# Optimization experiments

Hardware: AMD Instinct MI355X
Metric: run time of the kernel (lower is better)

Reference implementation:

```python
import jax, jax.numpy as jnp
import numpy as np
import itertools

N_SUBSETS = 4
TAU = 0.1


def setup_inputs() -> dict:
    key = jax.random.key(0)
    k1, k2, k3 = jax.random.split(key, 3)
    # scale projections so exp(sim/tau) stays numerically sane (module assumes small/normalized projections)
    projections = jax.random.normal(k1, (8192, 128), dtype=jnp.float32) * 0.05
    xrecon = jax.random.normal(k2, (8192, 784), dtype=jnp.float32)
    recon_label = jax.random.normal(k3, (8192, 784), dtype=jnp.float32)
    return {"projections": projections, "xrecon": xrecon, "recon_label": recon_label}


def _joint_loss(projections, xrecon, recon_label):
    # reconstruction MSE
    recon_loss = jnp.mean(jnp.square(xrecon - recon_label))

    # ---- XNegloss (SimCLR-style with n_subsets positives per group) ----
    N, D = projections.shape
    sim = (projections @ projections.T) / TAU  # [N, N] dot similarity
    gid = jnp.arange(N) // N_SUBSETS
    pos_mask = gid[:, None] == gid[None, :]  # same-group entries are positives
    exp_sim = jnp.exp(sim)
    # original code drops positive entries exactly equal to 1 (positives[positives != 1])
    pos_sum = jnp.sum(jnp.where(pos_mask & (sim != 1.0), exp_sim, 0.0), axis=-1)
    neg_sum = jnp.sum(jnp.where(pos_mask, 0.0, exp_sim), axis=-1)
    closs = jnp.mean(-jnp.log(pos_sum / (pos_sum + neg_sum)))

    # ---- distance loss: MSE over all subset pairs within each group ----
    combi = np.array(list(itertools.combinations(range(N_SUBSETS), 2)))
    left, right = combi[:, 0], combi[:, 1]
    P = projections.reshape(N // N_SUBSETS, N_SUBSETS, D)
    # per-group mean over (pairs, D) then mean over groups == global mean (equal counts)
    dist_loss = jnp.mean(jnp.square(P[:, left] - P[:, right]))

    loss = recon_loss + closs + dist_loss
    return loss, closs, recon_loss, dist_loss


def reference(projections, xrecon, recon_label):
    return _joint_loss(projections, xrecon, recon_label)
```

## Files before the change

### kernel.cpp

```cpp
#include <hip/hip_runtime.h>
#include <hip/hip_bf16.h>
#include <stdint.h>

typedef __bf16 bf16x8 __attribute__((ext_vector_type(8)));
typedef float  f32x4  __attribute__((ext_vector_type(4)));

#define NROWS   8192
#define DIMK    128
#define NGROUPS 2048
#define RECON_N 6422528
#define RECON_N4 (RECON_N / 4)
#define SIM_BLOCKS   512
#define RECON_BLOCKS 1568
#define GROUP_BLOCKS (NGROUPS / 4)
#define FUSED_BLOCKS (SIM_BLOCKS + RECON_BLOCKS + GROUP_BLOCKS)
#define CLOSS_BLOCKS 32

#define LOG2E10 14.4269504088896341f

#define WS_SP     0
#define WS_G      65536
#define WS_E      73728
#define WS_RPART  81920
#define WS_DPART  83488
#define WS_CPART  84000
#define WS_PB     84032

__device__ __forceinline__ unsigned short f2bf(float f) {
    union { __hip_bfloat16 h; unsigned short u; } v;
    v.h = __float2bfloat16(f);
    return v.u;
}

__global__ __launch_bounds__(256) void convert_kernel(const float4* __restrict__ P,
                                                      uint2* __restrict__ out) {
    int idx = blockIdx.x * 256 + threadIdx.x;
    float4 a = P[idx];
    uint2 r;
    r.x = (uint32_t)f2bf(a.x) | ((uint32_t)f2bf(a.y) << 16);
    r.y = (uint32_t)f2bf(a.z) | ((uint32_t)f2bf(a.w) << 16);
    out[idx] = r;
}

__global__ __launch_bounds__(256, 2) void fused_kernel(
        const unsigned short* __restrict__ Pb,
        const float* __restrict__ Pf,
        const float4* __restrict__ X,
        const float4* __restrict__ Y,
        float* __restrict__ ws) {
    const int bx = blockIdx.x;
    const int wave = threadIdx.x >> 6, lane = threadIdx.x & 63;

    if (bx < SIM_BLOCKS) {
        float* Sp = ws + WS_SP;
        __shared__ float sred[2][2][64];
        const int wr = wave >> 1, wc = wave & 1;
        const int rowBase = (bx >> 3) * 128;
        const int colBase = (bx & 7) * 1024;
        const int m = lane & 15, kq = lane >> 4;

        bf16x8 Af[4][4];
#pragma unroll
        for (int i = 0; i < 4; ++i) {
            const unsigned short* rowp =
                Pb + (size_t)(rowBase + wr * 64 + i * 16 + m) * DIMK + kq * 8;
#pragma unroll
            for (int kk = 0; kk < 4; ++kk)
                Af[i][kk] = *(const bf16x8*)(rowp + kk * 32);
        }

        float rowAcc[4][4];
#pragma unroll
        for (int i = 0; i < 4; ++i)
#pragma unroll
            for (int r = 0; r < 4; ++r) rowAcc[i][r] = 0.f;

        for (int t = 0; t < 8; ++t) {
            const unsigned short* bbase =
                Pb + (size_t)(colBase + t * 128 + wc * 64) * DIMK;
#pragma unroll
            for (int j = 0; j < 4; ++j) {
                const unsigned short* bp = bbase + (j * 16 + m) * DIMK + kq * 8;
                bf16x8 Bf[4];
#pragma unroll
                for (int kk = 0; kk < 4; ++kk)
                    Bf[kk] = *(const bf16x8*)(bp + kk * 32);
                f32x4 acc[4];
#pragma unroll
                for (int i = 0; i < 4; ++i) acc[i] = (f32x4){0.f, 0.f, 0.f, 0.f};
#pragma unroll
                for (int kk = 0; kk < 4; ++kk)
#pragma unroll
                    for (int i = 0; i < 4; ++i)
                        acc[i] = __builtin_amdgcn_mfma_f32_16x16x32_bf16(
                            Af[i][kk], Bf[kk], acc[i], 0, 0, 0);
#pragma unroll
                for (int i = 0; i < 4; ++i)
#pragma unroll
                    for (int r = 0; r < 4; ++r)
                        rowAcc[i][r] += exp2f(acc[i][r] * LOG2E10);
            }
        }

#pragma unroll
        for (int i = 0; i < 4; ++i)
#pragma unroll
            for (int r = 0; r < 4; ++r) {
                float sv = rowAcc[i][r];
                sv += __shfl_xor(sv, 1, 64);
                sv += __shfl_xor(sv, 2, 64);
                sv += __shfl_xor(sv, 4, 64);
                sv += __shfl_xor(sv, 8, 64);
                rowAcc[i][r] = sv;
            }
        if ((lane & 15) == 0) {
            int c = lane >> 4;
#pragma unroll
            for (int i = 0; i < 4; ++i)
#pragma unroll
                for (int r = 0; r < 4; ++r)
                    sred[wc][wr][i * 16 + c * 4 + r] = rowAcc[i][r];
        }
        __syncthreads();
        if (wc == 0) {
            float v = sred[0][wr][lane] + sred[1][wr][lane];
            Sp[(size_t)(bx & 7) * NROWS + rowBase + wr * 64 + lane] = v;
        }
    } else if (bx < SIM_BLOCKS + RECON_BLOCKS) {
        __shared__ float red[4];
        int rb = bx - SIM_BLOCKS;
        int base = rb * 1024 + threadIdx.x;
        float4 a0 = X[base], b0 = Y[base];
        float4 a1 = X[base + 256], b1 = Y[base + 256];
        float4 a2 = X[base + 512], b2 = Y[base + 512];
        float4 a3 = X[base + 768], b3 = Y[base + 768];
        float s = 0.f;
        float d;
        d = a0.x - b0.x; s += d * d;  d = a0.y - b0.y; s += d * d;
        d = a0.z - b0.z; s += d * d;  d = a0.w - b0.w; s += d * d;
        d = a1.x - b1.x; s += d * d;  d = a1.y - b1.y; s += d * d;
        d = a1.z - b1.z; s += d * d;  d = a1.w - b1.w; s += d * d;
        d = a2.x - b2.x; s += d * d;  d = a2.y - b2.y; s += d * d;
        d = a2.z - b2.z; s += d * d;  d = a2.w - b2.w; s += d * d;
        d = a3.x - b3.x; s += d * d;  d = a3.y - b3.y; s += d * d;
        d = a3.z - b3.z; s += d * d;  d = a3.w - b3.w; s += d * d;
#pragma unroll
        for (int mm = 1; mm < 64; mm <<= 1) s += __shfl_xor(s, mm, 64);
        if (lane == 0) red[wave] = s;
        __syncthreads();
        if (threadIdx.x == 0)
            ws[WS_RPART + rb] = red[0] + red[1] + red[2] + red[3];
    } else {
        __shared__ float dred[4];
        float* G = ws + WS_G;
        float* E = ws + WS_E;
        int gb = bx - (SIM_BLOCKS + RECON_BLOCKS);
        int g = gb * 4 + wave;
        const float* base = Pf + (size_t)g * 4 * DIMK;
        float v[4][2];
#pragma unroll
        for (int r = 0; r < 4; ++r) {
            v[r][0] = base[r * DIMK + lane];
            v[r][1] = base[r * DIMK + 64 + lane];
        }
        float dmat[4][4];
#pragma unroll
        for (int r = 0; r < 4; ++r)
#pragma unroll
            for (int s2 = r; s2 < 4; ++s2) {
                float p = v[r][0] * v[s2][0] + v[r][1] * v[s2][1];
#pragma unroll
                for (int mm = 1; mm < 64; mm <<= 1) p += __shfl_xor(p, mm, 64);
                dmat[r][s2] = p; dmat[s2][r] = p;
            }
        if (lane == 0) {
            float distp = 0.f;
#pragma unroll
            for (int r = 0; r < 4; ++r)
#pragma unroll
                for (int s2 = r + 1; s2 < 4; ++s2)
                    distp += dmat[r][r] + dmat[s2][s2] - 2.f * dmat[r][s2];
            dred[wave] = distp;
#pragma unroll
            for (int r = 0; r < 4; ++r) {
                float Gs = 0.f, Es = 0.f;
#pragma unroll
                for (int s2 = 0; s2 < 4; ++s2) {
                    float sim = dmat[r][s2] * 10.0f;
                    float e = __expf(sim);
                    Gs += e;
                    if (sim == 1.0f) Es += e;
                }
                G[g * 4 + r] = Gs;
                E[g * 4 + r] = Es;
            }
        }
        __syncthreads();
        if (threadIdx.x == 0)
            ws[WS_DPART + gb] = dred[0] + dred[1] + dred[2] + dred[3];
    }
}

__global__ __launch_bounds__(256) void closs_kernel(const float* __restrict__ ws,
                                                    float* __restrict__ cpart) {
    __shared__ float red[4];
    const float* Sp = ws + WS_SP;
    const float* G  = ws + WS_G;
    const float* E  = ws + WS_E;
    int r = blockIdx.x * 256 + threadIdx.x;
    float Sv = 0.f;
#pragma unroll
    for (int q = 0; q < 8; ++q) Sv += Sp[q * NROWS + r];
    float c = __logf(Sv - E[r]) - __logf(G[r] - E[r]);
#pragma unroll
    for (int m = 1; m < 64; m <<= 1) c += __shfl_xor(c, m, 64);
    int wave = threadIdx.x >> 6, lane = threadIdx.x & 63;
    if (lane == 0) red[wave] = c;
    __syncthreads();
    if (threadIdx.x == 0)
        cpart[blockIdx.x] = red[0] + red[1] + red[2] + red[3];
}

__global__ __launch_bounds__(256) void combine_kernel(const float* __restrict__ ws,
                                                      float* __restrict__ out) {
    __shared__ float redc[4], redr[4], redd[4];
    float cs = 0.f, rs = 0.f, ds = 0.f;
    for (int i = threadIdx.x; i < CLOSS_BLOCKS; i += 256) cs += ws[WS_CPART + i];
    for (int i = threadIdx.x; i < RECON_BLOCKS; i += 256) rs += ws[WS_RPART + i];
    for (int i = threadIdx.x; i < GROUP_BLOCKS; i += 256) ds += ws[WS_DPART + i];
#pragma unroll
    for (int m = 1; m < 64; m <<= 1) {
        cs += __shfl_xor(cs, m, 64);
        rs += __shfl_xor(rs, m, 64);
        ds += __shfl_xor(ds, m, 64);
    }
    int wave = threadIdx.x >> 6, lane = threadIdx.x & 63;
    if (lane == 0) { redc[wave] = cs; redr[wave] = rs; redd[wave] = ds; }
    __syncthreads();
    if (threadIdx.x == 0) {
        float closs = (redc[0] + redc[1] + redc[2] + redc[3]) / (float)NROWS;
        float recon = (redr[0] + redr[1] + redr[2] + redr[3]) / (float)RECON_N;
        float dist  = (redd[0] + redd[1] + redd[2] + redd[3]) / (float)(NGROUPS * 6 * DIMK);
        out[0] = recon + closs + dist;
        out[1] = closs;
        out[2] = recon;
        out[3] = dist;
    }
}

extern "C" void kernel_launch(void* const* d_in, const int* in_sizes, int n_in,
                              void* d_out, int out_size, void* d_ws, size_t ws_size,
                              hipStream_t stream) {
    const float* P  = (const float*)d_in[0];
    const float4* X = (const float4*)d_in[1];
    const float4* Y = (const float4*)d_in[2];
    float* out = (float*)d_out;
    float* w = (float*)d_ws;
    unsigned short* Pb = (unsigned short*)(w + WS_PB);

    convert_kernel<<<NROWS * DIMK / 4 / 256, 256, 0, stream>>>((const float4*)P, (uint2*)Pb);
    fused_kernel<<<FUSED_BLOCKS, 256, 0, stream>>>(Pb, P, X, Y, w);
    closs_kernel<<<CLOSS_BLOCKS, 256, 0, stream>>>(w, w + WS_CPART);
    combine_kernel<<<1, 256, 0, stream>>>(w, out);
}
```

Baseline: 126.2 us.

## Stage GEMM tiles in LDS via async loads and interleave block roles

The similarity GEMM blocks now load each 128x128 bf16 tile of the row and column operands into shared memory with global_load_lds async copies, then read MFMA fragments from LDS. Each B fragment is reused across four A fragments per k-step. Before this, every wave fetched B fragments straight from global memory. Block indices are also interleaved so that sim, recon and group blocks are mixed across the grid, balancing compute-heavy and bandwidth-heavy work per CU. The trade-offs are a 32KB LDS tile that lowers occupancy, two barriers per tile iteration with no double buffering, and possible LDS bank conflicts from the unpadded 256-byte row stride.

```diff
diff --git a/kernel.cpp b/kernel.cpp
--- a/kernel.cpp
+++ b/kernel.cpp
@@ -9,14 +9,11 @@
 #define DIMK    128
 #define NGROUPS 2048
 #define RECON_N 6422528
-#define RECON_N4 (RECON_N / 4)
 #define SIM_BLOCKS   512
 #define RECON_BLOCKS 1568
 #define GROUP_BLOCKS (NGROUPS / 4)
 #define FUSED_BLOCKS (SIM_BLOCKS + RECON_BLOCKS + GROUP_BLOCKS)
 #define CLOSS_BLOCKS 32
-
-#define LOG2E10 14.4269504088896341f
 
 #define WS_SP     0
 #define WS_G      65536
@@ -25,6 +22,12 @@
 #define WS_DPART  83488
 #define WS_CPART  84000
 #define WS_PB     84032
+
+__device__ __forceinline__ void async16(const void* g, void* l) {
+    __builtin_amdgcn_global_load_lds(
+        (const __attribute__((address_space(1))) void*)g,
+        (__attribute__((address_space(3))) void*)l, 16, 0, 0);
+}
 
 __device__ __forceinline__ unsigned short f2bf(float f) {
     union { __hip_bfloat16 h; unsigned short u; } v;
@@ -51,23 +54,46 @@
     const int bx = blockIdx.x;
     const int wave = threadIdx.x >> 6, lane = threadIdx.x & 63;
 
-    if (bx < SIM_BLOCKS) {
+    int role, idx;
+    if (bx < 2560) {
+        int r5 = bx % 5, c5 = bx / 5;
+        if (r5 == 0)      { role = 0; idx = c5; }
+        else if (r5 == 4) { role = 2; idx = c5; }
+        else              { role = 1; idx = c5 * 3 + (r5 - 1); }
+    } else {
+        role = 1; idx = 1536 + (bx - 2560);
+    }
+
+    if (role == 0) {
+        __shared__ unsigned short tile[128 * 128];
+        __shared__ float sred[2][2][64];
         float* Sp = ws + WS_SP;
-        __shared__ float sred[2][2][64];
         const int wr = wave >> 1, wc = wave & 1;
-        const int rowBase = (bx >> 3) * 128;
-        const int colBase = (bx & 7) * 1024;
-        const int m = lane & 15, kq = lane >> 4;
+        const int rowBase = (idx >> 3) * 128;
+        const int colBase = (idx & 7) * 1024;
+
+        {
+            const char* g = (const char*)(Pb + (size_t)rowBase * DIMK);
+#pragma unroll
+            for (int i = 0; i < 8; ++i) {
+                int seg = i * 4 + wave;
+                async16(g + seg * 1024 + lane * 16, (char*)tile + seg * 1024);
+            }
+        }
+        __syncthreads();
 
         bf16x8 Af[4][4];
-#pragma unroll
-        for (int i = 0; i < 4; ++i) {
-            const unsigned short* rowp =
-                Pb + (size_t)(rowBase + wr * 64 + i * 16 + m) * DIMK + kq * 8;
-#pragma unroll
-            for (int kk = 0; kk < 4; ++kk)
-                Af[i][kk] = *(const bf16x8*)(rowp + kk * 32);
-        }
+        {
+            int m = lane & 15, kq = lane >> 4;
+#pragma unroll
+            for (int i = 0; i < 4; ++i) {
+                const unsigned short* rowp = tile + (wr * 64 + i * 16 + m) * 128 + kq * 8;
+#pragma unroll
+                for (int kk = 0; kk < 4; ++kk)
+                    Af[i][kk] = *(const bf16x8*)(rowp + kk * 32);
+            }
+        }
+        __syncthreads();
 
         float rowAcc[4][4];
 #pragma unroll
@@ -76,30 +102,44 @@
             for (int r = 0; r < 4; ++r) rowAcc[i][r] = 0.f;
 
         for (int t = 0; t < 8; ++t) {
-            const unsigned short* bbase =
-                Pb + (size_t)(colBase + t * 128 + wc * 64) * DIMK;
-#pragma unroll
-            for (int j = 0; j < 4; ++j) {
-                const unsigned short* bp = bbase + (j * 16 + m) * DIMK + kq * 8;
+            {
+                const char* g = (const char*)(Pb + (size_t)(colBase + t * 128) * DIMK);
+#pragma unroll
+                for (int i = 0; i < 8; ++i) {
+                    int seg = i * 4 + wave;
+                    async16(g + seg * 1024 + lane * 16, (char*)tile + seg * 1024);
+                }
+            }
+            __syncthreads();
+
+            f32x4 acc[4][4];
+#pragma unroll
+            for (int i = 0; i < 4; ++i)
+#pragma unroll
+                for (int j = 0; j < 4; ++j) acc[i][j] = (f32x4){0.f, 0.f, 0.f, 0.f};
+
+            int n = lane & 15, kq = lane >> 4;
+#pragma unroll
+            for (int kk = 0; kk < 4; ++kk) {
                 bf16x8 Bf[4];
 #pragma unroll
-                for (int kk = 0; kk < 4; ++kk)
-                    Bf[kk] = *(const bf16x8*)(bp + kk * 32);
-                f32x4 acc[4];
-#pragma unroll
-                for (int i = 0; i < 4; ++i) acc[i] = (f32x4){0.f, 0.f, 0.f, 0.f};
-#pragma unroll
-                for (int kk = 0; kk < 4; ++kk)
-#pragma unroll
-                    for (int i = 0; i < 4; ++i)
-                        acc[i] = __builtin_amdgcn_mfma_f32_16x16x32_bf16(
-                            Af[i][kk], Bf[kk], acc[i], 0, 0, 0);
+                for (int j = 0; j < 4; ++j)
+                    Bf[j] = *(const bf16x8*)(tile + (wc * 64 + j * 16 + n) * 128 + kq * 8 + kk * 32);
 #pragma unroll
                 for (int i = 0; i < 4; ++i)
 #pragma unroll
+                    for (int j = 0; j < 4; ++j)
+                        acc[i][j] = __builtin_amdgcn_mfma_f32_16x16x32_bf16(
+                            Af[i][kk], Bf[j], acc[i][j], 0, 0, 0);
+            }
+#pragma unroll
+            for (int i = 0; i < 4; ++i)
+#pragma unroll
+                for (int j = 0; j < 4; ++j)
+#pragma unroll
                     for (int r = 0; r < 4; ++r)
-                        rowAcc[i][r] += exp2f(acc[i][r] * LOG2E10);
-            }
+                        rowAcc[i][r] += __expf(acc[i][j][r] * 10.0f);
+            __syncthreads();
         }
 
 #pragma unroll
@@ -124,18 +164,16 @@
         __syncthreads();
         if (wc == 0) {
             float v = sred[0][wr][lane] + sred[1][wr][lane];
-            Sp[(size_t)(bx & 7) * NROWS + rowBase + wr * 64 + lane] = v;
-        }
-    } else if (bx < SIM_BLOCKS + RECON_BLOCKS) {
+            Sp[(size_t)(idx & 7) * NROWS + rowBase + wr * 64 + lane] = v;
+        }
+    } else if (role == 1) {
         __shared__ float red[4];
-        int rb = bx - SIM_BLOCKS;
-        int base = rb * 1024 + threadIdx.x;
+        int base = idx * 1024 + threadIdx.x;
         float4 a0 = X[base], b0 = Y[base];
         float4 a1 = X[base + 256], b1 = Y[base + 256];
         float4 a2 = X[base + 512], b2 = Y[base + 512];
         float4 a3 = X[base + 768], b3 = Y[base + 768];
-        float s = 0.f;
-        float d;
+        float s = 0.f, d;
         d = a0.x - b0.x; s += d * d;  d = a0.y - b0.y; s += d * d;
         d = a0.z - b0.z; s += d * d;  d = a0.w - b0.w; s += d * d;
         d = a1.x - b1.x; s += d * d;  d = a1.y - b1.y; s += d * d;
@@ -149,13 +187,12 @@
         if (lane == 0) red[wave] = s;
         __syncthreads();
         if (threadIdx.x == 0)
-            ws[WS_RPART + rb] = red[0] + red[1] + red[2] + red[3];
+            ws[WS_RPART + idx] = red[0] + red[1] + red[2] + red[3];
     } else {
         __shared__ float dred[4];
         float* G = ws + WS_G;
         float* E = ws + WS_E;
-        int gb = bx - (SIM_BLOCKS + RECON_BLOCKS);
-        int g = gb * 4 + wave;
+        int g = idx * 4 + wave;
         const float* base = Pf + (size_t)g * 4 * DIMK;
         float v[4][2];
 #pragma unroll
@@ -197,7 +234,7 @@
         }
         __syncthreads();
         if (threadIdx.x == 0)
-            ws[WS_DPART + gb] = dred[0] + dred[1] + dred[2] + dred[3];
+            ws[WS_DPART + idx] = dred[0] + dred[1] + dred[2] + dred[3];
     }
 }
 
```

Result: slower. 134.2 us (+6.4%).
